# Optimization experiments

Measured on AMD Instinct MI355X. Metric: run time of the kernel, lower is better.

The kernel has to match this reference:

```python
import jax, jax.numpy as jnp
import numpy as np

# hyperparameters (module defaults)
T, B, N = 200, 64, 4096
TAU = 20.0
DT = 1.0
ETA = 0.1
NOISE_STD = 0.1
V_RESET = 0.0
MIN_TH = 0.5
MAX_TH = 2.0
ADAPT_DECAY = 0.9
SPIKE_INC = 0.5
DEP_RATE = 0.1
REC_RATE = 0.05


def setup_inputs() -> dict:
    key = jax.random.key(0)
    input_data = jax.random.normal(key, (T, B, N), dtype=jnp.float32)
    return {
        "input_data": input_data,
        "V0": jnp.zeros((B, N), jnp.float32),
        "V_th0": jnp.ones((B, N), jnp.float32),
        "adaptation0": jnp.zeros((B, N), jnp.float32),
        "syn_eff0": jnp.ones((B, N), jnp.float32),
        "neuromod0": jnp.zeros((B, N), jnp.float32),
    }


def _run(input_data, V0, V_th0, adaptation0, syn_eff0, neuromod0):
    # Deterministic per-step PRNG keys for noise + Bernoulli spike sampling.
    keys = jax.random.split(jax.random.key(42), input_data.shape[0])

    def step(carry, xs):
        V, Vth, adapt, syn = carry
        I, k = xs
        k_noise, k_spike = jax.random.split(k)
        noise = jax.random.normal(k_noise, I.shape, I.dtype) * NOISE_STD
        # effective input current with synaptic efficiency, neuromodulation, adaptation
        I_eff = I * syn + neuromod0 - adapt
        V = V + (I_eff - V) * (DT / TAU) + noise
        # stochastic spiking: sigmoid probability, Bernoulli sample
        spike_prob = jax.nn.sigmoid(V - Vth)
        spikes = jax.random.uniform(k_spike, V.shape, V.dtype) < spike_prob
        V = jnp.where(spikes, V_RESET, V)
        # adaptive threshold: bump on spike, relax toward 1.0 otherwise
        Vth = jnp.where(spikes, Vth + ETA, Vth - ETA * (Vth - 1.0))
        Vth = jnp.clip(Vth, MIN_TH, MAX_TH)
        sf = spikes.astype(V.dtype)
        adapt = adapt * ADAPT_DECAY + SPIKE_INC * sf
        syn = syn * (1.0 - DEP_RATE * sf) + REC_RATE * (1.0 - syn)
        return (V, Vth, adapt, syn), (spikes, V)

    _, (out_spikes, voltages) = jax.lax.scan(
        step, (V0, V_th0, adaptation0, syn_eff0), (input_data, keys)
    )
    return out_spikes, voltages  # (T,B,N) bool, (T,B,N) float


def reference(input_data, V0, V_th0, adaptation0, syn_eff0, neuromod0):
    return _run(input_data, V0, V_th0, adaptation0, syn_eff0, neuromod0)
```

## Files before the change

kernel.cpp:

```cpp
#include <hip/hip_runtime.h>
#include <stdint.h>


#define TSTEPS 200
#define BN     262144u
#define TBN    ((size_t)TSTEPS * (size_t)BN)

__device__ __forceinline__ void tf2x32(uint32_t k0, uint32_t k1,
                                       uint32_t c0, uint32_t c1,
                                       uint32_t& o0, uint32_t& o1) {
  uint32_t ks2 = k0 ^ k1 ^ 0x1BD11BDAu;
  uint32_t x0 = c0 + k0, x1 = c1 + k1;
#define R1(r) { x0 += x1; x1 = (x1 << (r)) | (x1 >> (32 - (r))); x1 ^= x0; }
#define R4A R1(13) R1(15) R1(26) R1(6)
#define R4B R1(17) R1(29) R1(16) R1(24)
  R4A; x0 += k1;  x1 += ks2 + 1u;
  R4B; x0 += ks2; x1 += k0 + 2u;
  R4A; x0 += k0;  x1 += k1 + 3u;
  R4B; x0 += k1;  x1 += ks2 + 4u;
  R4A; x0 += ks2; x1 += k0 + 5u;
#undef R4A
#undef R4B
#undef R1
  o0 = x0; o1 = x1;
}

__device__ __forceinline__ float erfinv_f32(float x) {
#pragma clang fp contract(off)
  float w = -log1pf(-(x * x));
  float p;
  if (w < 5.0f) {
    w = w - 2.5f;
    p =  2.81022636e-08f;
    p =  3.43273939e-07f + p * w;
    p = -3.5233877e-06f  + p * w;
    p = -4.39150654e-06f + p * w;
    p =  0.00021858087f  + p * w;
    p = -0.00125372503f  + p * w;
    p = -0.00417768164f  + p * w;
    p =  0.246640727f    + p * w;
    p =  1.50140941f     + p * w;
  } else {
    w = sqrtf(w) - 3.0f;
    p = -0.000200214257f;
    p =  0.000100950558f + p * w;
    p =  0.00134934322f  + p * w;
    p = -0.00367342844f  + p * w;
    p =  0.00573950773f  + p * w;
    p = -0.0076224613f   + p * w;
    p =  0.00943887047f  + p * w;
    p =  1.00167406f     + p * w;
    p =  2.83297682f     + p * w;
  }
  return p * x;
}

__device__ __forceinline__ float u01(uint32_t b) {
#pragma clang fp contract(off)
  return __uint_as_float((b >> 9) | 0x3f800000u) - 1.0f;
}

__global__ void keys_kernel(uint4* __restrict__ gK) {
  int t = blockIdx.x * blockDim.x + threadIdx.x;
  if (t >= TSTEPS) return;
  uint32_t K0, K1; tf2x32(0u, 42u, 0u, (uint32_t)t, K0, K1);
  uint32_t n0, n1; tf2x32(K0, K1, 0u, 0u, n0, n1);
  uint32_t s0, s1; tf2x32(K0, K1, 0u, 1u, s0, s1);
  gK[t] = make_uint4(n0, n1, s0, s1);
}

__global__ __launch_bounds__(256) void gen_kernel(
    const uint4* __restrict__ gK, float* __restrict__ gOut)
{
#pragma clang fp contract(off)
  const uint32_t t = blockIdx.y;
  const uint32_t e = blockIdx.x * 256u + threadIdx.x;

  uint4 kk = gK[t];
  uint32_t k0 = __builtin_amdgcn_readfirstlane(kk.x);
  uint32_t k1 = __builtin_amdgcn_readfirstlane(kk.y);
  uint32_t k2 = __builtin_amdgcn_readfirstlane(kk.z);
  uint32_t k3 = __builtin_amdgcn_readfirstlane(kk.w);

  const float LO = -0x1.fffffep-1f;
  const float SQRT2 = 1.4142135623730951f;

  uint32_t b0, b1; tf2x32(k0, k1, 0u, e, b0, b1);
  float un = u01(b0 ^ b1);
  float x = un * 2.0f + LO;
  x = fmaxf(LO, x);
  float noise = (SQRT2 * erfinv_f32(x)) * 0.1f;

  uint32_t c0, c1; tf2x32(k2, k3, 0u, e, c0, c1);
  float us = fmaxf(0.0f, u01(c0 ^ c1));

  size_t off = (size_t)t * BN + e;
  gOut[off] = noise;
  gOut[TBN + off] = us;
}

__global__ __launch_bounds__(256) void scan_kernel(
    const float* __restrict__ gI,
    const float* __restrict__ gV0, const float* __restrict__ gT0,
    const float* __restrict__ gA0, const float* __restrict__ gS0,
    const float* __restrict__ gN0,
    float* gOut)
{
#pragma clang fp contract(off)
  const uint32_t e = blockIdx.x * 256u + threadIdx.x;

  float V  = gV0[e];
  float Th = gT0[e];
  float Ad = gA0[e];
  float Sy = gS0[e];
  float Nm = gN0[e];

  const float* Ip = gI + e;
  float* Op = gOut + e;
  float* Up = gOut + TBN + e;

  float I0 = Ip[0],          N0 = Op[0],          U0 = Up[0];
  float I1 = Ip[(size_t)BN], N1 = Op[(size_t)BN], U1 = Up[(size_t)BN];

  for (int t = 0; t < TSTEPS; ++t) {
    float I2 = 0.0f, N2 = 0.0f, U2 = 0.0f;
    if (t + 2 < TSTEPS) {
      size_t pf = (size_t)(t + 2) * BN;
      I2 = Ip[pf]; N2 = Op[pf]; U2 = Up[pf];
    }

    float Ieff = (I0 * Sy + Nm) - Ad;
    V = (V + (Ieff - V) * 0.05f) + N0;
    float md = Th - V;
    float ex = expf(md);
    float p = 1.0f / (1.0f + ex);
    bool spk = U0 < p;
    float sf = spk ? 1.0f : 0.0f;

    V = spk ? 0.0f : V;
    float thn = Th - 0.1f * (Th - 1.0f);
    Th = spk ? (Th + 0.1f) : thn;
    Th = fminf(fmaxf(Th, 0.5f), 2.0f);
    Ad = Ad * 0.9f + 0.5f * sf;
    Sy = Sy * (1.0f - 0.1f * sf) + 0.05f * (1.0f - Sy);

    size_t so = (size_t)t * BN;
    __builtin_nontemporal_store(sf, Op + so);
    __builtin_nontemporal_store(V,  Up + so);

    I0 = I1; N0 = N1; U0 = U1;
    I1 = I2; N1 = N2; U1 = U2;
  }
}

extern "C" void kernel_launch(void* const* d_in, const int* in_sizes, int n_in,
                              void* d_out, int out_size, void* d_ws, size_t ws_size,
                              hipStream_t stream) {
  const float* I    = (const float*)d_in[0];
  const float* V0   = (const float*)d_in[1];
  const float* Vth0 = (const float*)d_in[2];
  const float* ad0  = (const float*)d_in[3];
  const float* sy0  = (const float*)d_in[4];
  const float* nm0  = (const float*)d_in[5];
  float* out = (float*)d_out;
  uint4* ktab = (uint4*)d_ws;

  keys_kernel<<<1, 256, 0, stream>>>(ktab);
  gen_kernel<<<dim3(BN / 256, TSTEPS), 256, 0, stream>>>(ktab, out);
  scan_kernel<<<BN / 256, 256, 0, stream>>>(I, V0, Vth0, ad0, sy0, nm0, out);
}
```

Baseline: 925.3 us.

## Fuse RNG generation into scan kernel, two neurons per thread

```diff
diff --git a/kernel.cpp b/kernel.cpp
--- a/kernel.cpp
+++ b/kernel.cpp
@@ -4,6 +4,7 @@
 
 #define TSTEPS 200
 #define BN     262144u
+#define HALF   131072u
 #define TBN    ((size_t)TSTEPS * (size_t)BN)
 
 __device__ __forceinline__ void tf2x32(uint32_t k0, uint32_t k1,
@@ -60,6 +61,44 @@
   return __uint_as_float((b >> 9) | 0x3f800000u) - 1.0f;
 }
 
+__device__ __forceinline__ float noise_from(uint32_t k0, uint32_t k1, uint32_t e) {
+#pragma clang fp contract(off)
+  const float LO = -0x1.fffffep-1f;
+  const float SQRT2 = 1.4142135623730951f;
+  uint32_t b0, b1; tf2x32(k0, k1, 0u, e, b0, b1);
+  float un = u01(b0 ^ b1);
+  float x = un * 2.0f + LO;
+  x = fmaxf(LO, x);
+  return (SQRT2 * erfinv_f32(x)) * 0.1f;
+}
+
+__device__ __forceinline__ float us_from(uint32_t k0, uint32_t k1, uint32_t e) {
+#pragma clang fp contract(off)
+  uint32_t c0, c1; tf2x32(k0, k1, 0u, e, c0, c1);
+  return fmaxf(0.0f, u01(c0 ^ c1));
+}
+
+struct LifState { float V, Th, Ad, Sy, Nm; };
+__device__ __forceinline__ void step_update(LifState& s, float I, float noise,
+                                            float us, float& sf_out, float& V_out) {
+#pragma clang fp contract(off)
+  float Ieff = (I * s.Sy + s.Nm) - s.Ad;
+  float V = (s.V + (Ieff - s.V) * 0.05f) + noise;
+  float md = s.Th - V;
+  float ex = expf(md);
+  float p = 1.0f / (1.0f + ex);
+  bool spk = us < p;
+  float sf = spk ? 1.0f : 0.0f;
+  V = spk ? 0.0f : V;
+  float thn = s.Th - 0.1f * (s.Th - 1.0f);
+  float Th = spk ? (s.Th + 0.1f) : thn;
+  s.Th = fminf(fmaxf(Th, 0.5f), 2.0f);
+  s.Ad = s.Ad * 0.9f + 0.5f * sf;
+  s.Sy = s.Sy * (1.0f - 0.1f * sf) + 0.05f * (1.0f - s.Sy);
+  s.V = V;
+  sf_out = sf; V_out = V;
+}
+
 __global__ void keys_kernel(uint4* __restrict__ gK) {
   int t = blockIdx.x * blockDim.x + threadIdx.x;
   if (t >= TSTEPS) return;
@@ -69,87 +108,61 @@
   gK[t] = make_uint4(n0, n1, s0, s1);
 }
 
-__global__ __launch_bounds__(256) void gen_kernel(
-    const uint4* __restrict__ gK, float* __restrict__ gOut)
-{
-#pragma clang fp contract(off)
-  const uint32_t t = blockIdx.y;
-  const uint32_t e = blockIdx.x * 256u + threadIdx.x;
-
-  uint4 kk = gK[t];
-  uint32_t k0 = __builtin_amdgcn_readfirstlane(kk.x);
-  uint32_t k1 = __builtin_amdgcn_readfirstlane(kk.y);
-  uint32_t k2 = __builtin_amdgcn_readfirstlane(kk.z);
-  uint32_t k3 = __builtin_amdgcn_readfirstlane(kk.w);
-
-  const float LO = -0x1.fffffep-1f;
-  const float SQRT2 = 1.4142135623730951f;
-
-  uint32_t b0, b1; tf2x32(k0, k1, 0u, e, b0, b1);
-  float un = u01(b0 ^ b1);
-  float x = un * 2.0f + LO;
-  x = fmaxf(LO, x);
-  float noise = (SQRT2 * erfinv_f32(x)) * 0.1f;
-
-  uint32_t c0, c1; tf2x32(k2, k3, 0u, e, c0, c1);
-  float us = fmaxf(0.0f, u01(c0 ^ c1));
-
-  size_t off = (size_t)t * BN + e;
-  gOut[off] = noise;
-  gOut[TBN + off] = us;
-}
-
-__global__ __launch_bounds__(256) void scan_kernel(
+__global__ __launch_bounds__(256) void lif2_kernel(
     const float* __restrict__ gI,
     const float* __restrict__ gV0, const float* __restrict__ gT0,
     const float* __restrict__ gA0, const float* __restrict__ gS0,
     const float* __restrict__ gN0,
-    float* gOut)
+    const uint4* __restrict__ gK,
+    float* __restrict__ gOut)
 {
 #pragma clang fp contract(off)
-  const uint32_t e = blockIdx.x * 256u + threadIdx.x;
+  const uint32_t e0 = blockIdx.x * 256u + threadIdx.x;
+  const uint32_t e1 = e0 + HALF;
 
-  float V  = gV0[e];
-  float Th = gT0[e];
-  float Ad = gA0[e];
-  float Sy = gS0[e];
-  float Nm = gN0[e];
+  LifState A = { gV0[e0], gT0[e0], gA0[e0], gS0[e0], gN0[e0] };
+  LifState Bs = { gV0[e1], gT0[e1], gA0[e1], gS0[e1], gN0[e1] };
 
-  const float* Ip = gI + e;
-  float* Op = gOut + e;
-  float* Up = gOut + TBN + e;
+  const float* Ipa = gI + e0;
+  const float* Ipb = gI + e1;
+  float* Soa = gOut + e0;
+  float* Sob = gOut + e1;
+  float* Voa = gOut + TBN + e0;
+  float* Vob = gOut + TBN + e1;
 
-  float I0 = Ip[0],          N0 = Op[0],          U0 = Up[0];
-  float I1 = Ip[(size_t)BN], N1 = Op[(size_t)BN], U1 = Up[(size_t)BN];
+  float I0a = Ipa[0],          I0b = Ipb[0];
+  float I1a = Ipa[(size_t)BN], I1b = Ipb[(size_t)BN];
 
   for (int t = 0; t < TSTEPS; ++t) {
-    float I2 = 0.0f, N2 = 0.0f, U2 = 0.0f;
+    float I2a = 0.0f, I2b = 0.0f;
     if (t + 2 < TSTEPS) {
       size_t pf = (size_t)(t + 2) * BN;
-      I2 = Ip[pf]; N2 = Op[pf]; U2 = Up[pf];
+      I2a = Ipa[pf]; I2b = Ipb[pf];
     }
 
-    float Ieff = (I0 * Sy + Nm) - Ad;
-    V = (V + (Ieff - V) * 0.05f) + N0;
-    float md = Th - V;
-    float ex = expf(md);
-    float p = 1.0f / (1.0f + ex);
-    bool spk = U0 < p;
-    float sf = spk ? 1.0f : 0.0f;
+    uint4 kk = gK[t];
+    uint32_t k0 = __builtin_amdgcn_readfirstlane(kk.x);
+    uint32_t k1 = __builtin_amdgcn_readfirstlane(kk.y);
+    uint32_t k2 = __builtin_amdgcn_readfirstlane(kk.z);
+    uint32_t k3 = __builtin_amdgcn_readfirstlane(kk.w);
 
-    V = spk ? 0.0f : V;
-    float thn = Th - 0.1f * (Th - 1.0f);
-    Th = spk ? (Th + 0.1f) : thn;
-    Th = fminf(fmaxf(Th, 0.5f), 2.0f);
-    Ad = Ad * 0.9f + 0.5f * sf;
-    Sy = Sy * (1.0f - 0.1f * sf) + 0.05f * (1.0f - Sy);
+    float na = noise_from(k0, k1, e0);
+    float nb = noise_from(k0, k1, e1);
+    float ua = us_from(k2, k3, e0);
+    float ub = us_from(k2, k3, e1);
+
+    float sfa, Va, sfb, Vb;
+    step_update(A,  I0a, na, ua, sfa, Va);
+    step_update(Bs, I0b, nb, ub, sfb, Vb);
 
     size_t so = (size_t)t * BN;
-    __builtin_nontemporal_store(sf, Op + so);
-    __builtin_nontemporal_store(V,  Up + so);
+    __builtin_nontemporal_store(sfa, Soa + so);
+    __builtin_nontemporal_store(sfb, Sob + so);
+    __builtin_nontemporal_store(Va,  Voa + so);
+    __builtin_nontemporal_store(Vb,  Vob + so);
 
-    I0 = I1; N0 = N1; U0 = U1;
-    I1 = I2; N1 = N2; U1 = U2;
+    I0a = I1a; I0b = I1b;
+    I1a = I2a; I1b = I2b;
   }
 }
 
@@ -166,6 +179,5 @@
   uint4* ktab = (uint4*)d_ws;
 
   keys_kernel<<<1, 256, 0, stream>>>(ktab);
-  gen_kernel<<<dim3(BN / 256, TSTEPS), 256, 0, stream>>>(ktab, out);
-  scan_kernel<<<BN / 256, 256, 0, stream>>>(I, V0, Vth0, ad0, sy0, nm0, out);
+  lif2_kernel<<<HALF / 256, 256, 0, stream>>>(I, V0, Vth0, ad0, sy0, nm0, ktab, out);
 }
```

Measured after the change: 856.9 us. 1.08x faster.
